# Kernel optimization log

Measured on AMD Instinct MI355X. Metric: run time of the kernel, lower is better.

Reference implementation:

```python
import jax, jax.numpy as jnp
import numpy as np

S, NB, C = 7, 2, 20
LAMBDA_COORD, LAMBDA_NOOBJ = 5.0, 0.5
EPS = 1e-6


def _iou(a, b):
    """Midpoint-format IoU. a, b: [..., 4] = (x, y, w, h)."""
    ax1, ay1 = a[..., 0] - a[..., 2] / 2, a[..., 1] - a[..., 3] / 2
    ax2, ay2 = a[..., 0] + a[..., 2] / 2, a[..., 1] + a[..., 3] / 2
    bx1, by1 = b[..., 0] - b[..., 2] / 2, b[..., 1] - b[..., 3] / 2
    bx2, by2 = b[..., 0] + b[..., 2] / 2, b[..., 1] + b[..., 3] / 2
    iw = jnp.clip(jnp.minimum(ax2, bx2) - jnp.maximum(ax1, bx1), 0.0)
    ih = jnp.clip(jnp.minimum(ay2, by2) - jnp.maximum(ay1, by1), 0.0)
    inter = iw * ih
    area_a = jnp.abs((ax2 - ax1) * (ay2 - ay1))
    area_b = jnp.abs((bx2 - bx1) * (by2 - by1))
    return inter / (area_a + area_b - inter + EPS)


def setup_inputs() -> dict:
    key = jax.random.key(0)
    k1, k2, k3, k4 = jax.random.split(key, 4)
    N = 16384
    predictions = jax.random.uniform(k1, (N, S * S * (C + NB * 5)), dtype=jnp.float32)
    cls = jax.random.uniform(k2, (N, S, S, C), dtype=jnp.float32)
    box_rest = jax.random.uniform(k3, (N, S, S, 4), dtype=jnp.float32)  # y,w,h,conf
    u = jax.random.uniform(k4, (N, S, S, 2), dtype=jnp.float32)
    flag = jnp.where(u[..., 0] < 0.3, 1.0, u[..., 1] * 0.99)
    targets = jnp.concatenate([cls, flag[..., None], box_rest], axis=-1)  # [N,S,S,25]
    return {"predictions": predictions, "targets": targets}


def reference(predictions, targets):
    N = predictions.shape[0]
    pred = predictions.reshape(N, S, S, C + NB * 5)
    class_pred = pred[..., :C]                      # [N,S,S,20]
    b1 = pred[..., C:C + 5]                         # [N,S,S,5]
    b2 = pred[..., C + 5:C + 10]                    # [N,S,S,5]
    tbox = targets[..., C:C + 5]                    # [N,S,S,5]
    obj = (targets[..., C] == 1.0).astype(pred.dtype)  # [N,S,S]

    iou1 = _iou(b1[..., :4], tbox[..., :4])
    iou2 = _iou(b2[..., :4], tbox[..., :4])
    resp = jnp.where((iou1 > iou2)[..., None], b1, b2)  # responsible box [N,S,S,5]

    xy = (resp[..., 0] - tbox[..., 0]) ** 2 + (resp[..., 1] - tbox[..., 1]) ** 2
    wh = (jnp.sqrt(resp[..., 2]) - jnp.sqrt(tbox[..., 2])) ** 2 \
       + (jnp.sqrt(resp[..., 3]) - jnp.sqrt(tbox[..., 3])) ** 2
    coord = LAMBDA_COORD * (xy + wh)
    conf = (resp[..., 4] - tbox[..., 4]) ** 2
    cls_loss = jnp.sum((class_pred - targets[..., :C]) ** 2, axis=-1)

    obj_terms = jnp.sum(obj * (coord + conf + cls_loss))
    noobj_terms = LAMBDA_NOOBJ * jnp.sum((1.0 - obj) * (b1[..., 4] ** 2 + b2[..., 4] ** 2))
    return (obj_terms + noobj_terms) / N
```

## Files before the change

### kernel.cpp

```cpp
#include <hip/hip_runtime.h>
#include <math.h>

#define SS 7
#define CC 20
#define CELL_PRED 30
#define CELL_TGT  25
#define TPB 256
#define WAVES 4
#define GRID 512
#define NW (GRID * WAVES)
#define REDUCE_BLOCK 256


#define PRED_TILE_B 7680
#define TGT_TILE_B  6400
#define TILE_FLOATS 3520

__device__ __forceinline__ void stage_tile_reg(const float* __restrict__ pred,
                                               const float* __restrict__ tgt,
                                               size_t t, float* lbuf, int lane)
{
    const float4* gp4 = (const float4*)((const char*)pred + t * (size_t)PRED_TILE_B);
    const float2* gp2 = (const float2*)gp4;
    const float4* gt4 = (const float4*)((const char*)tgt  + t * (size_t)TGT_TILE_B);
    const float*  gt1 = (const float*)gt4;

    float4 rp[7];
    #pragma unroll
    for (int k = 0; k < 7; ++k) rp[k] = gp4[k * 64 + lane];
    float2 rpt = gp2[896 + lane];
    float4 rt[6];
    #pragma unroll
    for (int k = 0; k < 6; ++k) rt[k] = gt4[k * 64 + lane];
    float  rtt = gt1[1536 + lane];

    float4* lp4 = (float4*)lbuf;
    #pragma unroll
    for (int k = 0; k < 7; ++k) lp4[k * 64 + lane] = rp[k];
    ((float2*)lbuf)[896 + lane] = rpt;
    float4* lt4 = (float4*)(lbuf + PRED_TILE_B / 4);
    #pragma unroll
    for (int k = 0; k < 6; ++k) lt4[k * 64 + lane] = rt[k];
    (lbuf + PRED_TILE_B / 4)[1536 + lane] = rtt;
}

__device__ __forceinline__ float cell_loss_ptr(const float* __restrict__ pc,
                                               const float* __restrict__ tc) {
    const float EPS = 1e-6f;
    float tv[CELL_TGT];
    #pragma unroll
    for (int j = 0; j < CELL_TGT; ++j) tv[j] = tc[j];

    const float2* p2 = (const float2*)pc;
    float cls = 0.0f;
    #pragma unroll
    for (int j = 0; j < 10; ++j) {
        float2 v = p2[j];
        float d0 = v.x - tv[2 * j];
        float d1 = v.y - tv[2 * j + 1];
        cls += d0 * d0;
        cls += d1 * d1;
    }
    float b[10];
    #pragma unroll
    for (int j = 0; j < 5; ++j) {
        float2 v = p2[10 + j];
        b[2 * j] = v.x; b[2 * j + 1] = v.y;
    }
    const float* b1 = b;
    const float* b2 = b + 5;
    const float* tb = tv + CC;

    float obj = (tb[0] == 1.0f) ? 1.0f : 0.0f;

    float t_x1 = tb[0] - tb[2] * 0.5f, t_y1 = tb[1] - tb[3] * 0.5f;
    float t_x2 = tb[0] + tb[2] * 0.5f, t_y2 = tb[1] + tb[3] * 0.5f;
    float t_area = fabsf((t_x2 - t_x1) * (t_y2 - t_y1));

    float a_x1 = b1[0] - b1[2] * 0.5f, a_y1 = b1[1] - b1[3] * 0.5f;
    float a_x2 = b1[0] + b1[2] * 0.5f, a_y2 = b1[1] + b1[3] * 0.5f;
    float iw1 = fmaxf(fminf(a_x2, t_x2) - fmaxf(a_x1, t_x1), 0.0f);
    float ih1 = fmaxf(fminf(a_y2, t_y2) - fmaxf(a_y1, t_y1), 0.0f);
    float inter1 = iw1 * ih1;
    float area1 = fabsf((a_x2 - a_x1) * (a_y2 - a_y1));
    float iou1 = inter1 / (area1 + t_area - inter1 + EPS);

    float c_x1 = b2[0] - b2[2] * 0.5f, c_y1 = b2[1] - b2[3] * 0.5f;
    float c_x2 = b2[0] + b2[2] * 0.5f, c_y2 = b2[1] + b2[3] * 0.5f;
    float iw2 = fmaxf(fminf(c_x2, t_x2) - fmaxf(c_x1, t_x1), 0.0f);
    float ih2 = fmaxf(fminf(c_y2, t_y2) - fmaxf(c_y1, t_y1), 0.0f);
    float inter2 = iw2 * ih2;
    float area2 = fabsf((c_x2 - c_x1) * (c_y2 - c_y1));
    float iou2 = inter2 / (area2 + t_area - inter2 + EPS);

    bool pick1 = iou1 > iou2;
    float r0 = pick1 ? b1[0] : b2[0];
    float r1 = pick1 ? b1[1] : b2[1];
    float r2 = pick1 ? b1[2] : b2[2];
    float r3 = pick1 ? b1[3] : b2[3];
    float r4 = pick1 ? b1[4] : b2[4];

    float dx = r0 - tb[0], dy = r1 - tb[1];
    float xy = dx * dx + dy * dy;
    float dw = sqrtf(r2) - sqrtf(tb[2]);
    float dh = sqrtf(r3) - sqrtf(tb[3]);
    float wh = dw * dw + dh * dh;
    float coord = 5.0f * (xy + wh);
    float dconf = r4 - tb[4];
    float conf = dconf * dconf;

    float noobj = 0.5f * (1.0f - obj) * (b1[4] * b1[4] + b2[4] * b2[4]);
    return obj * (coord + conf + cls) + noobj;
}

__global__ __launch_bounds__(TPB) void yolo_stream(
    const float* __restrict__ pred,
    const float* __restrict__ tgt,
    float* __restrict__ partials,
    int nCells)
{
    __shared__ __align__(16) float lds[WAVES][TILE_FLOATS];
    __shared__ float s_red[WAVES];
    const int tid  = threadIdx.x;
    const int lane = tid & 63;
    const int wid  = tid >> 6;
    const int gw   = blockIdx.x * WAVES + wid;
    const int nTiles = nCells >> 6;

    float* buf = lds[wid];
    float loss = 0.0f;

    const int myT = (gw < nTiles) ? ((nTiles - gw - 1) / NW + 1) : 0;
    size_t t = (size_t)gw;
    for (int i = 0; i < myT; ++i, t += NW) {
        stage_tile_reg(pred, tgt, t, buf, lane);
        loss += cell_loss_ptr(buf + lane * CELL_PRED,
                              buf + (PRED_TILE_B / 4) + lane * CELL_TGT);
    }

    if (gw == 0) {
        for (int c = (nTiles << 6) + lane; c < nCells; c += 64)
            loss += cell_loss_ptr(pred + (size_t)c * CELL_PRED,
                                  tgt  + (size_t)c * CELL_TGT);
    }

    #pragma unroll
    for (int off = 32; off > 0; off >>= 1)
        loss += __shfl_down(loss, off, 64);
    if (lane == 0) s_red[wid] = loss;
    __syncthreads();
    if (tid == 0)
        partials[blockIdx.x] = (s_red[0] + s_red[1]) + (s_red[2] + s_red[3]);
}

__global__ __launch_bounds__(REDUCE_BLOCK) void yolo_final_reduce(
    const float* __restrict__ partials, int nPartials, double invN,
    float* __restrict__ out)
{
    __shared__ double s_red[4];
    const float4* p4 = (const float4*)partials;
    double sum = 0.0;
    for (int i = threadIdx.x; i < (nPartials >> 2); i += REDUCE_BLOCK) {
        float4 v = p4[i];
        sum += (double)v.x + (double)v.y + (double)v.z + (double)v.w;
    }
    for (int i = ((nPartials >> 2) << 2) + threadIdx.x; i < nPartials; i += REDUCE_BLOCK)
        sum += (double)partials[i];
    #pragma unroll
    for (int off = 32; off > 0; off >>= 1)
        sum += __shfl_down(sum, off, 64);
    if ((threadIdx.x & 63) == 0) s_red[threadIdx.x >> 6] = sum;
    __syncthreads();
    if (threadIdx.x == 0) {
        double s = (s_red[0] + s_red[1]) + (s_red[2] + s_red[3]);
        out[0] = (float)(s * invN);
    }
}

extern "C" void kernel_launch(void* const* d_in, const int* in_sizes, int n_in,
                              void* d_out, int out_size, void* d_ws, size_t ws_size,
                              hipStream_t stream) {
    const float* pred = (const float*)d_in[0];
    const float* tgt  = (const float*)d_in[1];
    float* out = (float*)d_out;
    float* partials = (float*)d_ws;

    const int N = in_sizes[0] / (SS * SS * CELL_PRED);
    const int nCells = N * SS * SS;

    yolo_stream<<<GRID, TPB, 0, stream>>>(pred, tgt, partials, nCells);
    yolo_final_reduce<<<1, REDUCE_BLOCK, 0, stream>>>(partials, GRID, 1.0 / (double)N, out);
}
```

Measured before the change: 196.2 us.

## Software-pipeline tile loads into registers while computing on the LDS tile

Restructures the streaming loop so the next tile's global loads are issued into registers before the current tile's loss is computed from LDS. A sched_barrier keeps the compiler from sinking those loads past the compute. The registers are written to LDS afterwards, overlapping memory latency with ALU work. It also adds a min-blocks hint of 2 to launch_bounds. This raises register pressure, since a whole tile is held in registers across the compute. The LDS write after compute relies on per-wave ordering, because each wave uses only its own buffer.

```diff
diff --git a/kernel.cpp b/kernel.cpp
--- a/kernel.cpp
+++ b/kernel.cpp
@@ -16,32 +16,39 @@
 #define TGT_TILE_B  6400
 #define TILE_FLOATS 3520
 
-__device__ __forceinline__ void stage_tile_reg(const float* __restrict__ pred,
-                                               const float* __restrict__ tgt,
-                                               size_t t, float* lbuf, int lane)
+struct TileRegs {
+    float4 rp[7];
+    float2 rpt;
+    float4 rt[6];
+    float  rtt;
+};
+
+__device__ __forceinline__ void load_tile(const float* __restrict__ pred,
+                                          const float* __restrict__ tgt,
+                                          size_t t, int lane, TileRegs& r)
 {
     const float4* gp4 = (const float4*)((const char*)pred + t * (size_t)PRED_TILE_B);
     const float2* gp2 = (const float2*)gp4;
     const float4* gt4 = (const float4*)((const char*)tgt  + t * (size_t)TGT_TILE_B);
     const float*  gt1 = (const float*)gt4;
-
-    float4 rp[7];
-    #pragma unroll
-    for (int k = 0; k < 7; ++k) rp[k] = gp4[k * 64 + lane];
-    float2 rpt = gp2[896 + lane];
-    float4 rt[6];
-    #pragma unroll
-    for (int k = 0; k < 6; ++k) rt[k] = gt4[k * 64 + lane];
-    float  rtt = gt1[1536 + lane];
-
+    #pragma unroll
+    for (int k = 0; k < 7; ++k) r.rp[k] = gp4[k * 64 + lane];
+    r.rpt = gp2[896 + lane];
+    #pragma unroll
+    for (int k = 0; k < 6; ++k) r.rt[k] = gt4[k * 64 + lane];
+    r.rtt = gt1[1536 + lane];
+}
+
+__device__ __forceinline__ void write_tile(float* lbuf, int lane, const TileRegs& r)
+{
     float4* lp4 = (float4*)lbuf;
     #pragma unroll
-    for (int k = 0; k < 7; ++k) lp4[k * 64 + lane] = rp[k];
-    ((float2*)lbuf)[896 + lane] = rpt;
+    for (int k = 0; k < 7; ++k) lp4[k * 64 + lane] = r.rp[k];
+    ((float2*)lbuf)[896 + lane] = r.rpt;
     float4* lt4 = (float4*)(lbuf + PRED_TILE_B / 4);
     #pragma unroll
-    for (int k = 0; k < 6; ++k) lt4[k * 64 + lane] = rt[k];
-    (lbuf + PRED_TILE_B / 4)[1536 + lane] = rtt;
+    for (int k = 0; k < 6; ++k) lt4[k * 64 + lane] = r.rt[k];
+    (lbuf + PRED_TILE_B / 4)[1536 + lane] = r.rtt;
 }
 
 __device__ __forceinline__ float cell_loss_ptr(const float* __restrict__ pc,
@@ -113,7 +120,7 @@
     return obj * (coord + conf + cls) + noobj;
 }
 
-__global__ __launch_bounds__(TPB) void yolo_stream(
+__global__ __launch_bounds__(TPB, 2) void yolo_stream(
     const float* __restrict__ pred,
     const float* __restrict__ tgt,
     float* __restrict__ partials,
@@ -131,11 +138,22 @@
     float loss = 0.0f;
 
     const int myT = (gw < nTiles) ? ((nTiles - gw - 1) / NW + 1) : 0;
-    size_t t = (size_t)gw;
-    for (int i = 0; i < myT; ++i, t += NW) {
-        stage_tile_reg(pred, tgt, t, buf, lane);
-        loss += cell_loss_ptr(buf + lane * CELL_PRED,
-                              buf + (PRED_TILE_B / 4) + lane * CELL_TGT);
+
+    if (myT > 0) {
+        TileRegs r;
+        size_t t = (size_t)gw;
+        load_tile(pred, tgt, t, lane, r);
+        write_tile(buf, lane, r);
+        for (int i = 0; i < myT; ++i) {
+            t += NW;
+            if (i + 1 < myT)
+                load_tile(pred, tgt, t, lane, r);
+            __builtin_amdgcn_sched_barrier(0);
+            loss += cell_loss_ptr(buf + lane * CELL_PRED,
+                                  buf + (PRED_TILE_B / 4) + lane * CELL_TGT);
+            if (i + 1 < myT)
+                write_tile(buf, lane, r);
+        }
     }
 
     if (gw == 0) {
```

Result: slower. 206.3 us (+5.1%).
